# Performance work log

Hardware: AMD Instinct MI355X
Metric: run time of the kernel (lower is better)

Reference implementation:

```python
import jax, jax.numpy as jnp
import numpy as np

N_NODES = 100000
N_EDGES = 1600000
IN_FEATS = 128
HID = 32
N_REL = 5
N_BASES = 2
N_PAIRS = 4096


def setup_inputs() -> dict:
    key = jax.random.key(0)
    ks = jax.random.split(key, 24)
    d = {}
    d['x'] = jax.random.normal(ks[0], (N_NODES, IN_FEATS), dtype=jnp.float32)
    d['edge_mask'] = jnp.ones((N_EDGES,), dtype=jnp.float32)
    d['etype'] = jax.random.randint(ks[1], (N_EDGES,), 0, N_REL, dtype=jnp.int32)
    d['src'] = jax.random.randint(ks[2], (N_EDGES,), 0, N_NODES, dtype=jnp.int32)
    d['dst'] = jax.random.randint(ks[3], (N_EDGES,), 0, N_NODES, dtype=jnp.int32)
    d['users_idx'] = jax.random.randint(ks[4], (N_PAIRS,), 0, N_NODES, dtype=jnp.int32)
    d['items_idx'] = jax.random.randint(ks[5], (N_PAIRS,), 0, N_NODES, dtype=jnp.int32)
    # RelGraphConv params (basis decomposition): layer1 in->32, layers 2,3 32->32
    def s(k, din):
        return 1.0 / np.sqrt(din)
    d['V1'] = jax.random.normal(ks[6], (N_BASES, IN_FEATS, HID), dtype=jnp.float32) * s(0, IN_FEATS)
    d['comp1'] = jax.random.normal(ks[7], (N_REL, N_BASES), dtype=jnp.float32)
    d['loop1'] = jax.random.normal(ks[8], (IN_FEATS, HID), dtype=jnp.float32) * s(0, IN_FEATS)
    d['b1'] = jnp.zeros((HID,), dtype=jnp.float32)
    d['V2'] = jax.random.normal(ks[9], (N_BASES, HID, HID), dtype=jnp.float32) * s(0, HID)
    d['comp2'] = jax.random.normal(ks[10], (N_REL, N_BASES), dtype=jnp.float32)
    d['loop2'] = jax.random.normal(ks[11], (HID, HID), dtype=jnp.float32) * s(0, HID)
    d['b2'] = jnp.zeros((HID,), dtype=jnp.float32)
    d['V3'] = jax.random.normal(ks[12], (N_BASES, HID, HID), dtype=jnp.float32) * s(0, HID)
    d['comp3'] = jax.random.normal(ks[13], (N_REL, N_BASES), dtype=jnp.float32)
    d['loop3'] = jax.random.normal(ks[14], (HID, HID), dtype=jnp.float32) * s(0, HID)
    d['b3'] = jnp.zeros((HID,), dtype=jnp.float32)
    # MLP head: lin1 (2*sum(latent_dim[1:]) = 192 -> 128), lin2 (128 -> 1)
    d['w1'] = jax.random.normal(ks[15], (2 * 3 * HID, 128), dtype=jnp.float32) * (1.0 / np.sqrt(2 * 3 * HID))
    d['bw1'] = jnp.zeros((128,), dtype=jnp.float32)
    d['w2'] = jax.random.normal(ks[16], (128, 1), dtype=jnp.float32) * (1.0 / np.sqrt(128))
    d['bw2'] = jnp.zeros((1,), dtype=jnp.float32)
    return d


def _rgcn_layer(x, V, comp, loopw, bias, etype, src, dst, norm):
    # basis-decomposed relational conv: W_r = sum_b comp[r,b] * V[b]
    xb = jnp.einsum('nd,bdo->nbo', x, V)                       # [N,B,O]
    msg = jnp.einsum('eb,ebo->eo', comp[etype], xb[src])       # [E,O]
    msg = msg * norm[:, None]                                  # edge_mask norm
    agg = jax.ops.segment_sum(msg, dst, num_segments=x.shape[0])
    return jnp.tanh(agg + x @ loopw + bias)


def reference(x, edge_mask, etype, src, dst, users_idx, items_idx,
              V1, comp1, loop1, b1, V2, comp2, loop2, b2, V3, comp3, loop3, b3,
              w1, bw1, w2, bw2):
    h1 = _rgcn_layer(x, V1, comp1, loop1, b1, etype, src, dst, edge_mask)
    h2 = _rgcn_layer(h1, V2, comp2, loop2, b2, etype, src, dst, edge_mask)
    h3 = _rgcn_layer(h2, V3, comp3, loop3, b3, etype, src, dst, edge_mask)
    concat_states = jnp.concatenate([h1, h2, h3], axis=1)      # [N, 96]
    feats = jnp.concatenate([concat_states[users_idx], concat_states[items_idx]], axis=1)  # [P,192]
    hidden = jax.nn.relu(feats @ w1 + bw1)
    out = hidden @ w2 + bw2
    return out[:, 0]  # multiply_by = 1
```

## Files before the change

### kernel.cpp

```cpp
#include <hip/hip_runtime.h>
#include <stdint.h>

#define N_NODES  100000
#define N_EDGES  1600000
#define IN_FEATS 128
#define HID      32
#define N_REL    5
#define N_BASES  2
#define N_PAIRS  4096

#define NB        196
#define BCAP      16384
#define EPB       2048
#define SC_BLOCKS 782
#define WP_BLOCKS 136
#define NBSORT    392
#define TD_BLOCKS 625

typedef __attribute__((ext_vector_type(8))) short short8;
typedef __attribute__((ext_vector_type(4))) float f32x4;

__device__ inline unsigned int pack_bf16(float a, float b) {
    unsigned int ua = __float_as_uint(a), ub = __float_as_uint(b);
    ua = (ua + 0x7fffu + ((ua >> 16) & 1u)) >> 16;
    ub = (ub + 0x7fffu + ((ub >> 16) & 1u)) >> 16;
    return ua | (ub << 16);
}

__device__ inline unsigned short bf16_1(float a) {
    unsigned int u = __float_as_uint(a);
    u = (u + 0x7fffu + ((u >> 16) & 1u)) >> 16;
    return (unsigned short)u;
}

__device__ inline void split_bf16_2(float a, float b, unsigned int& hi, unsigned int& lo) {
    unsigned int ha = bf16_1(a), hb = bf16_1(b);
    hi = ha | (hb << 16);
    float fa = __uint_as_float(ha << 16), fb = __uint_as_float(hb << 16);
    lo = pack_bf16(a - fa, b - fb);
}


#define SMEM_BYTES 23856

__global__ __launch_bounds__(256) void k_scatter_wprep(
    const int* __restrict__ src, const int* __restrict__ dst,
    const int* __restrict__ etype, const float* __restrict__ mask,
    int* __restrict__ gcur, int2* __restrict__ ebuf,
    const float* __restrict__ V1, const float* __restrict__ comp1, const float* __restrict__ loop1,
    const float* __restrict__ V2, const float* __restrict__ loop2,
    const float* __restrict__ V3, const float* __restrict__ loop3,
    unsigned short* __restrict__ Wbf1, unsigned short* __restrict__ Wcat2,
    unsigned short* __restrict__ Wcat3) {
    __shared__ __attribute__((aligned(16))) char smem[SMEM_BYTES];
    int b = blockIdx.x;
    int t = threadIdx.x;
    if (b < SC_BLOCKS) {
        int2*  srec    = (int2*)smem;
        short* sb      = (short*)(smem + 16384);
        int*   lh      = (int*)(smem + 20480);
        int*   lex     = (int*)(smem + 21264);
        int*   gbase   = (int*)(smem + 22048);
        int*   scanbuf = (int*)(smem + 22832);
        int e0 = b * EPB;
        if (t < NB) lh[t] = 0;
        __syncthreads();
        int2 rec[8];
        int  bk[8];
#pragma unroll
        for (int i = 0; i < 8; i++) {
            int e = e0 + t + i * 256;
            if (e < N_EDGES) {
                int d = dst[e];
                bk[i] = d >> 9;
                rec[i].x = ((d & 511) << 23) | (src[e] << 4) | etype[e];
                rec[i].y = __float_as_int(mask[e]);
                atomicAdd(&lh[bk[i]], 1);
            } else bk[i] = -1;
        }
        __syncthreads();
        int cnt = (t < NB) ? lh[t] : 0;
        scanbuf[t] = cnt;
        __syncthreads();
        for (int off = 1; off < 256; off <<= 1) {
            int v = (t >= off) ? scanbuf[t - off] : 0;
            __syncthreads();
            scanbuf[t] += v;
            __syncthreads();
        }
        if (t < NB) {
            lex[t] = scanbuf[t] - cnt;
            gbase[t] = t * BCAP + (cnt ? atomicAdd(&gcur[t], cnt) : 0);
            lh[t] = 0;
        }
        __syncthreads();
#pragma unroll
        for (int i = 0; i < 8; i++) {
            if (bk[i] >= 0) {
                int p = lex[bk[i]] + atomicAdd(&lh[bk[i]], 1);
                srec[p] = rec[i];
                sb[p] = (short)bk[i];
            }
        }
        __syncthreads();
        int total = scanbuf[NB - 1];
        for (int idx = t; idx < total; idx += 256) {
            int bb = sb[idx];
            ebuf[gbase[bb] + (idx - lex[bb])] = srec[idx];
        }
        return;
    }
    int wb = b - SC_BLOCKS;
    if (wb < 96) {
        int idx = wb * 256 + t;
        if (idx >= 192 * IN_FEATS) return;
        int j = idx / IN_FEATS, k = idx % IN_FEATS;
        float v;
        if (j < 160) {
            int r = j >> 5, o = j & 31;
            v = comp1[r * 2 + 0] * V1[(size_t)(0 * IN_FEATS + k) * 32 + o]
              + comp1[r * 2 + 1] * V1[(size_t)(1 * IN_FEATS + k) * 32 + o];
        } else {
            v = loop1[k * 32 + (j - 160)];
        }
        Wbf1[idx] = bf16_1(v);
        return;
    }
    const float *V, *loopw;
    unsigned short* Wc;
    int idx;
    if (wb < 116) { V = V2; loopw = loop2; Wc = Wcat2; idx = (wb - 96) * 256 + t; }
    else          { V = V3; loopw = loop3; Wc = Wcat3; idx = (wb - 116) * 256 + t; }
    if (idx >= 32 * 160) return;
    int col = idx / 160, k = idx % 160;
    int seg = k >> 5, inner = k & 31;
    float v;
    if (seg < 2)      v = V[inner * 32 + col];
    else if (seg < 4) v = V[(32 + inner) * 32 + col];
    else              v = loopw[inner * 32 + col];
    Wc[idx] = bf16_1(v);
}


#define SMEM2_BYTES 19456

__global__ __launch_bounds__(512) void k_bsort_tl1(
    const int* __restrict__ gcur, const int2* __restrict__ ebuf,
    int2* __restrict__ esort, int* __restrict__ offsets,
    const float* __restrict__ xin,
    const unsigned short* __restrict__ Wbf, const float* __restrict__ bias,
    unsigned short* __restrict__ xs16, float* __restrict__ aggout) {
    __shared__ __attribute__((aligned(16))) char smem2[SMEM2_BYTES];
    int b = blockIdx.x;
    int t = threadIdx.x;
    if (b < NBSORT) {
        int* hist = (int*)smem2;
        int* incl = (int*)(smem2 + 2048);
        int* cur  = (int*)(smem2 + 4096);
        int* bs   = (int*)(smem2 + 6144);
        int* sBC  = (int*)(smem2 + 7168);
        int bb = b >> 1, h = b & 1;
        if (t < 256) bs[t] = (t < NB) ? gcur[t] : 0;
        __syncthreads();
        for (int off = 1; off < 256; off <<= 1) {
            int v = 0;
            if (t < 256 && t >= off) v = bs[t - off];
            __syncthreads();
            if (t < 256) bs[t] += v;
            __syncthreads();
        }
        if (t == 0) { sBC[1] = gcur[bb]; sBC[0] = bs[bb] - gcur[bb]; }
        hist[t] = 0;
        __syncthreads();
        int cnt = sBC[1], gbase = sBC[0];
        const int2* slab = ebuf + (size_t)bb * BCAP;
        for (int e = t; e < cnt; e += 512) {
            int dl = ((unsigned)slab[e].x) >> 23;
            atomicAdd(&hist[dl], 1);
        }
        __syncthreads();
        incl[t] = hist[t];
        __syncthreads();
        for (int off = 1; off < 512; off <<= 1) {
            int v = 0;
            if (t >= off) v = incl[t - off];
            __syncthreads();
            incl[t] += v;
            __syncthreads();
        }
        int ex = incl[t] - hist[t];
        cur[t] = ex;
        if ((t >> 8) == h) {
            int n = (bb << 9) + t;
            if (n <= N_NODES) offsets[n] = gbase + ex;
        }
        if (bb == NB - 1 && h == 1 && t == 0) offsets[N_NODES] = N_EDGES;
        __syncthreads();
        for (int e = t; e < cnt; e += 512) {
            int2 pk = slab[e];
            int dl = ((unsigned)pk.x) >> 23;
            if ((dl >> 8) == h) {
                int pos = gbase + atomicAdd(&cur[dl], 1);
                int2 rec;
                rec.x = pk.x & 0x7fffff;
                rec.y = pk.y;
                esort[pos] = rec;
            }
        }
        return;
    }
    int half = t >> 8;
    int tl   = t & 255;
    char* basep = smem2 + half * 9728;
    unsigned short* As = (unsigned short*)basep;
    unsigned short* tb = (unsigned short*)(basep + 4352);
    int bb = (b - NBSORT) * 2 + half;
    int wv = tl >> 6, lane = tl & 63;
    int q = lane >> 4, n16 = lane & 15;
    short8 bfr[3][4];
#pragma unroll
    for (int i = 0; i < 3; i++) {
        int tt = wv * 3 + i;
#pragma unroll
        for (int ks = 0; ks < 4; ks++)
            bfr[i][ks] = *(const short8*)(Wbf + (tt * 16 + n16) * 128 + ks * 32 + q * 8);
    }
    float bv0 = bias[n16], bv1 = bias[16 + n16];
    int node_l = tl >> 4;
    int seg    = tl & 15;
    int g0 = bb * 5;
    float4 p0, p1;
    {
        const float* xr = xin + ((size_t)(g0 * 16 + node_l)) * 128 + seg * 8;
        p0 = *(const float4*)xr;
        p1 = *(const float4*)(xr + 4);
    }
    for (int gi = 0; gi < 5; gi++) {
        int g = g0 + gi;
        int n0 = g * 16;
        __syncthreads();
        {
            uint4 v;
            v.x = pack_bf16(p0.x, p0.y);
            v.y = pack_bf16(p0.z, p0.w);
            v.z = pack_bf16(p1.x, p1.y);
            v.w = pack_bf16(p1.z, p1.w);
            *(uint4*)(As + node_l * 136 + seg * 8) = v;
        }
        __syncthreads();
        if (gi + 1 < 5) {
            const float* xr = xin + ((size_t)((g + 1) * 16 + node_l)) * 128 + seg * 8;
            p0 = *(const float4*)xr;
            p1 = *(const float4*)(xr + 4);
        }
        short8 afr[4];
#pragma unroll
        for (int ks = 0; ks < 4; ks++)
            afr[ks] = *(const short8*)(As + n16 * 136 + ks * 32 + q * 8);
        f32x4 d[3];
        f32x4 z = {0.f, 0.f, 0.f, 0.f};
#pragma unroll
        for (int i = 0; i < 3; i++) d[i] = z;
#pragma unroll
        for (int i = 0; i < 3; i++)
#pragma unroll
            for (int ks = 0; ks < 4; ks++)
                d[i] = __builtin_amdgcn_mfma_f32_16x16x32_bf16(afr[ks], bfr[i][ks], d[i], 0, 0, 0);
#pragma unroll
        for (int i = 0; i < 3; i++) {
            int tt = wv * 3 + i;
            if (tt < 10) {
#pragma unroll
                for (int r = 0; r < 4; r++)
                    tb[(q * 4 + r) * 168 + tt * 16 + n16] = bf16_1(d[i][r]);
            } else {
                float bv = (tt == 10) ? bv0 : bv1;
                int o = (tt - 10) * 16 + n16;
#pragma unroll
                for (int r = 0; r < 4; r++) {
                    int node = n0 + q * 4 + r;
                    aggout[(size_t)node * 32 + o] = d[i][r] + bv;
                }
            }
        }
        __syncthreads();
        for (int c = tl; c < 320; c += 256) {
            int node_i = c / 20, part = c % 20;
            short8 vv = *(const short8*)(tb + node_i * 168 + part * 8);
            *(short8*)(xs16 + (size_t)(n0 + node_i) * 160 + part * 8) = vv;
        }
    }
}


__global__ __launch_bounds__(256) void k_agg1(
    const int* __restrict__ offsets, const int2* __restrict__ esort,
    const unsigned int* __restrict__ xrel16, const float* __restrict__ agg,
    float* __restrict__ concat, unsigned int* __restrict__ hrel_out) {
    int v = blockIdx.x * 32 + (threadIdx.x >> 3);
    int o = threadIdx.x & 7;
    int s0 = offsets[v], s1 = offsets[v + 1];
    float4 a0 = *(const float4*)(agg + (size_t)v * 32 + o * 4);
    float acc0 = a0.x, acc1 = a0.y, acc2 = a0.z, acc3 = a0.w;
    int last = s1 - 1;
    for (int e = s0; e < s1; e += 16) {
        int addr[16];
        float m[16];
#pragma unroll
        for (int i = 0; i < 16; i++) {
            int ei = e + i;
            int ec = (ei <= last) ? ei : last;
            int2 pk = esort[ec];
            int low = pk.x;
            addr[i] = (low >> 4) * 80 + (low & 15) * 16;
            m[i] = (ei <= last) ? __int_as_float(pk.y) : 0.f;
        }
        uint2 xw[16];
#pragma unroll
        for (int i = 0; i < 16; i++)
            xw[i] = *(const uint2*)(xrel16 + (unsigned)addr[i] + o * 2);
#pragma unroll
        for (int i = 0; i < 16; i++) {
            float f0 = __uint_as_float(xw[i].x << 16);
            float f1 = __uint_as_float(xw[i].x & 0xffff0000u);
            float f2 = __uint_as_float(xw[i].y << 16);
            float f3 = __uint_as_float(xw[i].y & 0xffff0000u);
            acc0 = fmaf(m[i], f0, acc0);
            acc1 = fmaf(m[i], f1, acc1);
            acc2 = fmaf(m[i], f2, acc2);
            acc3 = fmaf(m[i], f3, acc3);
        }
    }
    float4 r;
    r.x = tanhf(acc0); r.y = tanhf(acc1); r.z = tanhf(acc2); r.w = tanhf(acc3);
    *(float4*)(concat + (size_t)v * 96 + o * 4) = r;
    hrel_out[v * 16 + o * 2]     = pack_bf16(r.x, r.y);
    hrel_out[v * 16 + o * 2 + 1] = pack_bf16(r.z, r.w);
}


__global__ __launch_bounds__(256) void k_agg23(
    const int* __restrict__ offsets, const int2* __restrict__ esort,
    const unsigned int* __restrict__ hrel_in, const float* __restrict__ comp,
    const unsigned short* __restrict__ Wcat, const float* __restrict__ bias,
    float* __restrict__ concat, int hoff, unsigned int* __restrict__ hrel_out) {
    __shared__ unsigned int hbf[32][84];
    __shared__ float2 cLds[5];
    int t = threadIdx.x;
    if (t < 5) cLds[t] = ((const float2*)comp)[t];
    int nl = t >> 3;
    int v = blockIdx.x * 32 + nl;
    int o = t & 7;
    int s0 = offsets[v], s1 = offsets[v + 1];
    __syncthreads();
    float y00 = 0.f, y01 = 0.f, y02 = 0.f, y03 = 0.f;
    float y10 = 0.f, y11 = 0.f, y12 = 0.f, y13 = 0.f;
    int last = s1 - 1;
    for (int e = s0; e < s1; e += 16) {
        int addr[16];
        float c0[16], c1[16];
#pragma unroll
        for (int i = 0; i < 16; i++) {
            int ei = e + i;
            int ec = (ei <= last) ? ei : last;
            int2 pk = esort[ec];
            int low = pk.x;
            addr[i] = low & 0x7ffff0;
            float2 cc = cLds[low & 15];
            float m = (ei <= last) ? __int_as_float(pk.y) : 0.f;
            c0[i] = m * cc.x;
            c1[i] = m * cc.y;
        }
        uint2 xw[16];
#pragma unroll
        for (int i = 0; i < 16; i++)
            xw[i] = *(const uint2*)(hrel_in + (unsigned)addr[i] + o * 2);
#pragma unroll
        for (int i = 0; i < 16; i++) {
            float f0 = __uint_as_float(xw[i].x << 16);
            float f1 = __uint_as_float(xw[i].x & 0xffff0000u);
            float f2 = __uint_as_float(xw[i].y << 16);
            float f3 = __uint_as_float(xw[i].y & 0xffff0000u);
            y00 = fmaf(c0[i], f0, y00); y10 = fmaf(c1[i], f0, y10);
            y01 = fmaf(c0[i], f1, y01); y11 = fmaf(c1[i], f1, y11);
            y02 = fmaf(c0[i], f2, y02); y12 = fmaf(c1[i], f2, y12);
            y03 = fmaf(c0[i], f3, y03); y13 = fmaf(c1[i], f3, y13);
        }
    }
    unsigned int hi, lo;
    split_bf16_2(y00, y01, hi, lo);
    hbf[nl][o * 2]          = hi;  hbf[nl][16 + o * 2]     = lo;
    split_bf16_2(y02, y03, hi, lo);
    hbf[nl][o * 2 + 1]      = hi;  hbf[nl][16 + o * 2 + 1] = lo;
    split_bf16_2(y10, y11, hi, lo);
    hbf[nl][32 + o * 2]     = hi;  hbf[nl][48 + o * 2]     = lo;
    split_bf16_2(y12, y13, hi, lo);
    hbf[nl][32 + o * 2 + 1] = hi;  hbf[nl][48 + o * 2 + 1] = lo;
    *(uint2*)&hbf[nl][64 + o * 2] = *(const uint2*)(hrel_in + v * 16 + o * 2);
    __syncthreads();
    int wv = t >> 6, lane = t & 63;
    int q = lane >> 4, n16 = lane & 15;
    int gg = wv & 1;
    int tt = wv >> 1;
    f32x4 d = {0.f, 0.f, 0.f, 0.f};
#pragma unroll
    for (int ks = 0; ks < 5; ks++) {
        short8 afr = *(const short8*)&hbf[gg * 16 + n16][ks * 16 + q * 4];
        short8 bfr = *(const short8*)(Wcat + (tt * 16 + n16) * 160 + ks * 32 + q * 8);
        d = __builtin_amdgcn_mfma_f32_16x16x32_bf16(afr, bfr, d, 0, 0, 0);
    }
    float bv = bias[tt * 16 + n16];
    int n0 = blockIdx.x * 32 + gg * 16;
#pragma unroll
    for (int r = 0; r < 4; r++) {
        int node = n0 + q * 4 + r;
        float h = tanhf(d[r] + bv);
        concat[(size_t)node * 96 + hoff + tt * 16 + n16] = h;
        if (hrel_out)
            ((unsigned short*)hrel_out)[node * 32 + tt * 16 + n16] = bf16_1(h);
    }
}


__global__ void k_mlp(const float* __restrict__ concat, const int* __restrict__ uidx,
                      const int* __restrict__ iidx,
                      const float* __restrict__ w1, const float* __restrict__ bw1,
                      const float* __restrict__ w2, const float* __restrict__ bw2,
                      float* __restrict__ out) {
    __shared__ float feats[192];
    __shared__ float red[2];
    int p = blockIdx.x;
    int t = threadIdx.x;
    int u = uidx[p], it = iidx[p];
    for (int k = t; k < 192; k += 128)
        feats[k] = (k < 96) ? concat[(size_t)u * 96 + k] : concat[(size_t)it * 96 + (k - 96)];
    __syncthreads();
    float acc = bw1[t];
    for (int k = 0; k < 192; k++) acc += feats[k] * w1[k * 128 + t];
    float h = fmaxf(acc, 0.f);
    float part = h * w2[t];
    for (int off = 32; off > 0; off >>= 1) part += __shfl_down(part, off, 64);
    if ((t & 63) == 0) red[t >> 6] = part;
    __syncthreads();
    if (t == 0) out[p] = red[0] + red[1] + bw2[0];
}


extern "C" void kernel_launch(void* const* d_in, const int* in_sizes, int n_in,
                              void* d_out, int out_size, void* d_ws, size_t ws_size,
                              hipStream_t stream) {
    const float* x         = (const float*)d_in[0];
    const float* edge_mask = (const float*)d_in[1];
    const int*   etype     = (const int*)d_in[2];
    const int*   src       = (const int*)d_in[3];
    const int*   dst       = (const int*)d_in[4];
    const int*   users_idx = (const int*)d_in[5];
    const int*   items_idx = (const int*)d_in[6];
    const float* V1        = (const float*)d_in[7];
    const float* comp1     = (const float*)d_in[8];
    const float* loop1     = (const float*)d_in[9];
    const float* b1        = (const float*)d_in[10];
    const float* V2        = (const float*)d_in[11];
    const float* comp2     = (const float*)d_in[12];
    const float* loop2     = (const float*)d_in[13];
    const float* b2        = (const float*)d_in[14];
    const float* V3        = (const float*)d_in[15];
    const float* comp3     = (const float*)d_in[16];
    const float* loop3     = (const float*)d_in[17];
    const float* b3        = (const float*)d_in[18];
    const float* w1        = (const float*)d_in[19];
    const float* bw1       = (const float*)d_in[20];
    const float* w2        = (const float*)d_in[21];
    const float* bw2       = (const float*)d_in[22];
    float* out = (float*)d_out;

    uintptr_t w = (uintptr_t)d_ws;
    auto al = [&](size_t bytes) { uintptr_t p = (w + 255) & ~(uintptr_t)255; w = p + bytes; return p; };
    int*   gcur    = (int*)al(sizeof(int) * NB);
    int*   offsets = (int*)al(sizeof(int) * (N_NODES + 1));
    int2*  ebuf    = (int2*)al(sizeof(int2) * (size_t)NB * BCAP);
    unsigned int* xs16  = (unsigned int*)al(sizeof(unsigned int) * (size_t)N_NODES * 80);
    unsigned int* hrel1 = (unsigned int*)al(sizeof(unsigned int) * (size_t)N_NODES * 16);
    unsigned int* hrel2 = (unsigned int*)al(sizeof(unsigned int) * (size_t)N_NODES * 16);
    int2*  esort   = (int2*)al(sizeof(int2) * N_EDGES);
    unsigned short* Wbf1  = (unsigned short*)al(sizeof(unsigned short) * 192 * IN_FEATS);
    unsigned short* Wcat2 = (unsigned short*)al(sizeof(unsigned short) * 32 * 160);
    unsigned short* Wcat3 = (unsigned short*)al(sizeof(unsigned short) * 32 * 160);
    float* aggA    = (float*)al(sizeof(float) * (size_t)N_NODES * 32);
    float* concat  = (float*)al(sizeof(float) * (size_t)N_NODES * 96);

    hipMemsetAsync(gcur, 0, sizeof(int) * NB, stream);

    k_scatter_wprep<<<SC_BLOCKS + WP_BLOCKS, 256, 0, stream>>>(
        src, dst, etype, edge_mask, gcur, ebuf,
        V1, comp1, loop1, V2, loop2, V3, loop3, Wbf1, Wcat2, Wcat3);
    k_bsort_tl1<<<NBSORT + TD_BLOCKS, 512, 0, stream>>>(
        gcur, ebuf, esort, offsets,
        x, Wbf1, b1, (unsigned short*)xs16, aggA);

    const int agrid = N_NODES / 32;

    k_agg1<<<agrid, 256, 0, stream>>>(offsets, esort, xs16, aggA, concat, hrel1);
    k_agg23<<<agrid, 256, 0, stream>>>(offsets, esort, hrel1, comp2, Wcat2, b2,
                                       concat, 32, hrel2);
    k_agg23<<<agrid, 256, 0, stream>>>(offsets, esort, hrel2, comp3, Wcat3, b3,
                                       concat, 64, (unsigned int*)nullptr);

    k_mlp<<<N_PAIRS, 128, 0, stream>>>(concat, users_idx, items_idx, w1, bw1, w2, bw2, out);
}
```

Measured before the change: 318.8 us.

## Compute layer-3 only for queried nodes and mask concat writes by flags

Layer 3 is now run only for the 8192 user and item nodes the MLP head reads, instead of all 100k nodes, using a new gather-style kernel over the pair indices. A flag array marking those nodes is built inside the prep kernel and used to skip the fp32 concat writes for all other nodes in layers 1 and 2. This removes most of the layer-3 edge aggregation work and most concat write traffic. It adds a flag load per node and a small flag-building block. Duplicate indices simply write the same values twice.

```diff
diff --git a/kernel.cpp b/kernel.cpp
--- a/kernel.cpp
+++ b/kernel.cpp
@@ -13,7 +13,7 @@
 #define BCAP      16384
 #define EPB       2048
 #define SC_BLOCKS 782
-#define WP_BLOCKS 136
+#define WP_BLOCKS 137
 #define NBSORT    392
 #define TD_BLOCKS 625
 
@@ -51,7 +51,9 @@
     const float* __restrict__ V2, const float* __restrict__ loop2,
     const float* __restrict__ V3, const float* __restrict__ loop3,
     unsigned short* __restrict__ Wbf1, unsigned short* __restrict__ Wcat2,
-    unsigned short* __restrict__ Wcat3) {
+    unsigned short* __restrict__ Wcat3,
+    const int* __restrict__ uidx, const int* __restrict__ iidx,
+    unsigned char* __restrict__ flags) {
     __shared__ __attribute__((aligned(16))) char smem[SMEM_BYTES];
     int b = blockIdx.x;
     int t = threadIdx.x;
@@ -111,6 +113,16 @@
         return;
     }
     int wb = b - SC_BLOCKS;
+    if (wb == 136) {
+        unsigned int* f4 = (unsigned int*)flags;
+        for (int i = t; i < 25000; i += 256) f4[i] = 0u;
+        __syncthreads();
+        for (int i = t; i < N_PAIRS; i += 256) {
+            flags[uidx[i]] = 1;
+            flags[iidx[i]] = 1;
+        }
+        return;
+    }
     if (wb < 96) {
         int idx = wb * 256 + t;
         if (idx >= 192 * IN_FEATS) return;
@@ -296,7 +308,8 @@
 __global__ __launch_bounds__(256) void k_agg1(
     const int* __restrict__ offsets, const int2* __restrict__ esort,
     const unsigned int* __restrict__ xrel16, const float* __restrict__ agg,
-    float* __restrict__ concat, unsigned int* __restrict__ hrel_out) {
+    float* __restrict__ concat, unsigned int* __restrict__ hrel_out,
+    const unsigned char* __restrict__ flags) {
     int v = blockIdx.x * 32 + (threadIdx.x >> 3);
     int o = threadIdx.x & 7;
     int s0 = offsets[v], s1 = offsets[v + 1];
@@ -333,7 +346,8 @@
     }
     float4 r;
     r.x = tanhf(acc0); r.y = tanhf(acc1); r.z = tanhf(acc2); r.w = tanhf(acc3);
-    *(float4*)(concat + (size_t)v * 96 + o * 4) = r;
+    if (flags[v])
+        *(float4*)(concat + (size_t)v * 96 + o * 4) = r;
     hrel_out[v * 16 + o * 2]     = pack_bf16(r.x, r.y);
     hrel_out[v * 16 + o * 2 + 1] = pack_bf16(r.z, r.w);
 }
@@ -343,7 +357,8 @@
     const int* __restrict__ offsets, const int2* __restrict__ esort,
     const unsigned int* __restrict__ hrel_in, const float* __restrict__ comp,
     const unsigned short* __restrict__ Wcat, const float* __restrict__ bias,
-    float* __restrict__ concat, int hoff, unsigned int* __restrict__ hrel_out) {
+    float* __restrict__ concat, int hoff, unsigned int* __restrict__ hrel_out,
+    const unsigned char* __restrict__ flags) {
     __shared__ unsigned int hbf[32][84];
     __shared__ float2 cLds[5];
     int t = threadIdx.x;
@@ -415,9 +430,97 @@
     for (int r = 0; r < 4; r++) {
         int node = n0 + q * 4 + r;
         float h = tanhf(d[r] + bv);
-        concat[(size_t)node * 96 + hoff + tt * 16 + n16] = h;
+        if (flags[node])
+            concat[(size_t)node * 96 + hoff + tt * 16 + n16] = h;
         if (hrel_out)
             ((unsigned short*)hrel_out)[node * 32 + tt * 16 + n16] = bf16_1(h);
+    }
+}
+
+
+__global__ __launch_bounds__(256) void k_agg3s(
+    const int* __restrict__ offsets, const int2* __restrict__ esort,
+    const unsigned int* __restrict__ hrel_in, const float* __restrict__ comp,
+    const unsigned short* __restrict__ Wcat, const float* __restrict__ bias,
+    const int* __restrict__ uidx, const int* __restrict__ iidx,
+    float* __restrict__ concat) {
+    __shared__ unsigned int hbf[32][84];
+    __shared__ float2 cLds[5];
+    __shared__ int nlist[32];
+    int t = threadIdx.x;
+    if (t < 5) cLds[t] = ((const float2*)comp)[t];
+    if (t < 32) {
+        int slot = blockIdx.x * 32 + t;
+        nlist[t] = (slot < N_PAIRS) ? uidx[slot] : iidx[slot - N_PAIRS];
+    }
+    __syncthreads();
+    int nl = t >> 3;
+    int v = nlist[nl];
+    int o = t & 7;
+    int s0 = offsets[v], s1 = offsets[v + 1];
+    float y00 = 0.f, y01 = 0.f, y02 = 0.f, y03 = 0.f;
+    float y10 = 0.f, y11 = 0.f, y12 = 0.f, y13 = 0.f;
+    int last = s1 - 1;
+    for (int e = s0; e < s1; e += 16) {
+        int addr[16];
+        float c0[16], c1[16];
+#pragma unroll
+        for (int i = 0; i < 16; i++) {
+            int ei = e + i;
+            int ec = (ei <= last) ? ei : last;
+            int2 pk = esort[ec];
+            int low = pk.x;
+            addr[i] = low & 0x7ffff0;
+            float2 cc = cLds[low & 15];
+            float m = (ei <= last) ? __int_as_float(pk.y) : 0.f;
+            c0[i] = m * cc.x;
+            c1[i] = m * cc.y;
+        }
+        uint2 xw[16];
+#pragma unroll
+        for (int i = 0; i < 16; i++)
+            xw[i] = *(const uint2*)(hrel_in + (unsigned)addr[i] + o * 2);
+#pragma unroll
+        for (int i = 0; i < 16; i++) {
+            float f0 = __uint_as_float(xw[i].x << 16);
+            float f1 = __uint_as_float(xw[i].x & 0xffff0000u);
+            float f2 = __uint_as_float(xw[i].y << 16);
+            float f3 = __uint_as_float(xw[i].y & 0xffff0000u);
+            y00 = fmaf(c0[i], f0, y00); y10 = fmaf(c1[i], f0, y10);
+            y01 = fmaf(c0[i], f1, y01); y11 = fmaf(c1[i], f1, y11);
+            y02 = fmaf(c0[i], f2, y02); y12 = fmaf(c1[i], f2, y12);
+            y03 = fmaf(c0[i], f3, y03); y13 = fmaf(c1[i], f3, y13);
+        }
+    }
+    unsigned int hi, lo;
+    split_bf16_2(y00, y01, hi, lo);
+    hbf[nl][o * 2]          = hi;  hbf[nl][16 + o * 2]     = lo;
+    split_bf16_2(y02, y03, hi, lo);
+    hbf[nl][o * 2 + 1]      = hi;  hbf[nl][16 + o * 2 + 1] = lo;
+    split_bf16_2(y10, y11, hi, lo);
+    hbf[nl][32 + o * 2]     = hi;  hbf[nl][48 + o * 2]     = lo;
+    split_bf16_2(y12, y13, hi, lo);
+    hbf[nl][32 + o * 2 + 1] = hi;  hbf[nl][48 + o * 2 + 1] = lo;
+    *(uint2*)&hbf[nl][64 + o * 2] = *(const uint2*)(hrel_in + v * 16 + o * 2);
+    __syncthreads();
+    int wv = t >> 6, lane = t & 63;
+    int q = lane >> 4, n16 = lane & 15;
+    int gg = wv & 1;
+    int tt = wv >> 1;
+    f32x4 d = {0.f, 0.f, 0.f, 0.f};
+#pragma unroll
+    for (int ks = 0; ks < 5; ks++) {
+        short8 afr = *(const short8*)&hbf[gg * 16 + n16][ks * 16 + q * 4];
+        short8 bfr = *(const short8*)(Wcat + (tt * 16 + n16) * 160 + ks * 32 + q * 8);
+        d = __builtin_amdgcn_mfma_f32_16x16x32_bf16(afr, bfr, d, 0, 0, 0);
+    }
+    float bv = bias[tt * 16 + n16];
+    int base = gg * 16 + q * 4;
+#pragma unroll
+    for (int r = 0; r < 4; r++) {
+        int node = nlist[base + r];
+        float h = tanhf(d[r] + bv);
+        concat[(size_t)node * 96 + 64 + tt * 16 + n16] = h;
     }
 }
 
@@ -477,6 +580,7 @@
     uintptr_t w = (uintptr_t)d_ws;
     auto al = [&](size_t bytes) { uintptr_t p = (w + 255) & ~(uintptr_t)255; w = p + bytes; return p; };
     int*   gcur    = (int*)al(sizeof(int) * NB);
+    unsigned char* flags = (unsigned char*)al(100000);
     int*   offsets = (int*)al(sizeof(int) * (N_NODES + 1));
     int2*  ebuf    = (int2*)al(sizeof(int2) * (size_t)NB * BCAP);
     unsigned int* xs16  = (unsigned int*)al(sizeof(unsigned int) * (size_t)N_NODES * 80);
@@ -493,18 +597,19 @@
 
     k_scatter_wprep<<<SC_BLOCKS + WP_BLOCKS, 256, 0, stream>>>(
         src, dst, etype, edge_mask, gcur, ebuf,
-        V1, comp1, loop1, V2, loop2, V3, loop3, Wbf1, Wcat2, Wcat3);
+        V1, comp1, loop1, V2, loop2, V3, loop3, Wbf1, Wcat2, Wcat3,
+        users_idx, items_idx, flags);
     k_bsort_tl1<<<NBSORT + TD_BLOCKS, 512, 0, stream>>>(
         gcur, ebuf, esort, offsets,
         x, Wbf1, b1, (unsigned short*)xs16, aggA);
 
     const int agrid = N_NODES / 32;
 
-    k_agg1<<<agrid, 256, 0, stream>>>(offsets, esort, xs16, aggA, concat, hrel1);
+    k_agg1<<<agrid, 256, 0, stream>>>(offsets, esort, xs16, aggA, concat, hrel1, flags);
     k_agg23<<<agrid, 256, 0, stream>>>(offsets, esort, hrel1, comp2, Wcat2, b2,
-                                       concat, 32, hrel2);
-    k_agg23<<<agrid, 256, 0, stream>>>(offsets, esort, hrel2, comp3, Wcat3, b3,
-                                       concat, 64, (unsigned int*)nullptr);
+                                       concat, 32, hrel2, flags);
+    k_agg3s<<<256, 256, 0, stream>>>(offsets, esort, hrel2, comp3, Wcat3, b3,
+                                     users_idx, items_idx, concat);
 
     k_mlp<<<N_PAIRS, 128, 0, stream>>>(concat, users_idx, items_idx, w1, bw1, w2, bw2, out);
 }
```

New measurement: 300.2 us (median of 2 runs). -5.8%, faster.
